# Performance work log

Hardware: AMD Instinct MI355X
Metric: run time of the kernel (lower is better)

## Reference

```python
import jax, jax.numpy as jnp
import numpy as np
from jax import lax

POINTS = 512  # number of FPS-sampled centroids
KNN = 16      # neighbors per centroid


def setup_inputs() -> dict:
    key = jax.random.key(0)
    # [B, N, 3+C]: first 3 channels are xyz coordinates, rest are features
    x = jax.random.normal(key, (8, 16384, 16), dtype=jnp.float32)
    return {"x": x}


def _furthest_point_sample(xyz, npoint):
    """Standard FPS (seeded at index 0, as in the pointnet2 CUDA op).
    xyz: [B, N, 3] -> idx: [B, npoint] int32."""
    B, N, _ = xyz.shape

    def step(carry, _):
        min_d, last = carry
        last_pt = jnp.take_along_axis(xyz, last[:, None, None], axis=1)  # [B,1,3]
        d = jnp.sum((xyz - last_pt) ** 2, axis=-1)                        # [B,N]
        min_d = jnp.minimum(min_d, d)
        nxt = jnp.argmax(min_d, axis=-1).astype(jnp.int32)
        return (min_d, nxt), nxt

    first = jnp.zeros((B,), dtype=jnp.int32)
    init = (jnp.full((B, N), 1e10, dtype=xyz.dtype), first)
    _, rest = lax.scan(step, init, None, length=npoint - 1)  # [npoint-1, B]
    return jnp.concatenate([first[:, None], rest.T], axis=1)  # [B, npoint]


def _index_points(points, idx):
    """points: [B,N,C], idx: [B,S] or [B,S,K] -> gathered [*idx.shape, C]."""
    B = points.shape[0]
    flat = idx.reshape(B, -1)                                  # [B, S*K]
    out = jnp.take_along_axis(points, flat[:, :, None], axis=1)
    return out.reshape(*idx.shape, points.shape[-1])


def reference(x):
    # FPS over coordinates only
    idx = _furthest_point_sample(x[:, :, :3], POINTS)          # [B, P]
    sampled = _index_points(x, idx)                             # [B, P, 3+C]
    s = sampled[:, :, :3]
    p = x[:, :, :3]
    # squared euclidean distance: ||s||^2 + ||p||^2 - 2 s.p  -> [B, P, N]
    dist = (jnp.sum(s * s, axis=-1)[:, :, None]
            + jnp.sum(p * p, axis=-1)[:, None, :]
            - 2.0 * jnp.einsum('bpc,bnc->bpn', s, p))
    # full argsort then slice, matching distances.argsort()[:, :, :knn]
    knn_idx = jnp.argsort(dist, axis=-1)[:, :, :KNN]            # [B, P, K]
    return _index_points(x, knn_idx)                            # [B, P, K, 3+C]
```

## Files before the change

kernel.cpp:

```cpp
#include <hip/hip_runtime.h>
#include <hip/hip_bf16.h>
#include <stdint.h>

#define B_      8
#define N_      16384
#define NPOINT  512
#define KNN_    16
#define C_      16

__device__ __forceinline__ float fmulrn(float a, float b){ return __fmul_rn(a,b); }
__device__ __forceinline__ float faddrn(float a, float b){ return __fadd_rn(a,b); }
__device__ __forceinline__ float fsubrn(float a, float b){ return __fsub_rn(a,b); }

__device__ __forceinline__ uint32_t umax_(uint32_t a, uint32_t b){ return a > b ? a : b; }

__device__ __forceinline__ uint32_t row16_max(uint32_t x){
    uint32_t t;
    t = (uint32_t)__builtin_amdgcn_update_dpp((int)x, (int)x, 0x111, 0xf, 0xf, false); x = umax_(x, t);
    t = (uint32_t)__builtin_amdgcn_update_dpp((int)x, (int)x, 0x112, 0xf, 0xf, false); x = umax_(x, t);
    t = (uint32_t)__builtin_amdgcn_update_dpp((int)x, (int)x, 0x114, 0xf, 0xf, false); x = umax_(x, t);
    t = (uint32_t)__builtin_amdgcn_update_dpp((int)x, (int)x, 0x118, 0xf, 0xf, false); x = umax_(x, t);
    return x;
}

__device__ __forceinline__ uint32_t wave_max_uniform(uint32_t x){
    x = row16_max(x);
    uint32_t a = (uint32_t)__builtin_amdgcn_readlane((int)x, 15);
    uint32_t b = (uint32_t)__builtin_amdgcn_readlane((int)x, 31);
    uint32_t c = (uint32_t)__builtin_amdgcn_readlane((int)x, 47);
    uint32_t d = (uint32_t)__builtin_amdgcn_readlane((int)x, 63);
    return umax_(umax_(a, b), umax_(c, d));
}

__device__ __forceinline__ unsigned long long quad_max_u64(unsigned long long k){
    uint32_t lo = (uint32_t)k, hi = (uint32_t)(k >> 32);
    {
        uint32_t olo = (uint32_t)__builtin_amdgcn_update_dpp((int)lo, (int)lo, 0xB1, 0xf, 0xf, false);
        uint32_t ohi = (uint32_t)__builtin_amdgcn_update_dpp((int)hi, (int)hi, 0xB1, 0xf, 0xf, false);
        bool take = (ohi > hi) || (ohi == hi && olo > lo);
        hi = take ? ohi : hi; lo = take ? olo : lo;
    }
    {
        uint32_t olo = (uint32_t)__builtin_amdgcn_update_dpp((int)lo, (int)lo, 0x4E, 0xf, 0xf, false);
        uint32_t ohi = (uint32_t)__builtin_amdgcn_update_dpp((int)hi, (int)hi, 0x4E, 0xf, 0xf, false);
        bool take = (ohi > hi) || (ohi == hi && olo > lo);
        hi = take ? ohi : hi; lo = take ? olo : lo;
    }
    return ((unsigned long long)hi << 32) | lo;
}

__global__ void prep_kernel(const float* __restrict__ x, float4* __restrict__ pts){
    int i = blockIdx.x * blockDim.x + threadIdx.x;
    if (i >= B_ * N_) return;
    const float4* x4 = (const float4*)x;
    float4 q = x4[(size_t)i * 4];
    float p2 = faddrn(faddrn(fmulrn(q.x,q.x), fmulrn(q.y,q.y)), fmulrn(q.z,q.z));
    pts[i] = make_float4(q.x, q.y, q.z, p2);
}

#define FPS_NB  4
__global__ void zero_part_kernel(unsigned long long* __restrict__ part){
    int i = blockIdx.x * blockDim.x + threadIdx.x;
    if (i < B_ * NPOINT * FPS_NB) part[i] = 0ULL;
}

#define FPS_T    1024
#define FPS_NW   (FPS_T/64)
#define SLICE    (N_ / FPS_NB)
#define SLOTS_MB (SLICE / FPS_T)

#define FOR_S4(F) F(0) F(1) F(2) F(3)

__global__ void __launch_bounds__(FPS_T)
fps_kernel_mb(const float4* __restrict__ pts, float4* __restrict__ s_out,
              unsigned long long* __restrict__ part){
    __shared__ float2   xy[SLICE];
    __shared__ uint32_t red_v[2][FPS_NW];
    __shared__ uint32_t red_i[2][FPS_NW];

    const int b    = blockIdx.x & 7;
    const int blk  = blockIdx.x >> 3;
    const int tid  = threadIdx.x;
    const int lane = tid & 63;
    const int wv   = tid >> 6;
    const int base = blk * SLICE;
    const float4* P = pts + (size_t)b * N_;
    unsigned long long* mbox = part + ((size_t)b * NPOINT) * FPS_NB;

#define DECL_S(s) float z##s, md##s;
    FOR_S4(DECL_S)
#undef DECL_S

#define INIT_S(s) { float4 q = P[base + (s) * FPS_T + tid]; \
        xy[(s) * FPS_T + tid] = make_float2(q.x, q.y); \
        z##s = q.z; md##s = 1e10f; }
    FOR_S4(INIT_S)
#undef INIT_S

    float lx, ly, lz;
    {
        float4 q0 = P[0];
        lx = q0.x; ly = q0.y; lz = q0.z;
        if (blk == 0 && tid == 0) s_out[(size_t)b * NPOINT + 0] = q0;
    }
    __syncthreads();

    for (int it = 1; it < NPOINT; ++it){
        float    bv = -1.0f;
        uint32_t bi = 0;
#define DO_S(s) { \
        float2 c = xy[(s) * FPS_T + tid]; \
        float dx = fsubrn(c.x, lx); \
        float dy = fsubrn(c.y, ly); \
        float dz = fsubrn(z##s, lz); \
        float d  = faddrn(faddrn(fmulrn(dx,dx), fmulrn(dy,dy)), fmulrn(dz,dz)); \
        md##s = fminf(md##s, d); \
        if (md##s > bv){ bv = md##s; bi = (uint32_t)(base + (s) * FPS_T + tid); } }
        FOR_S4(DO_S)
#undef DO_S

        uint32_t vb    = __float_as_uint(bv);
        uint32_t gmaxw = wave_max_uniform(vb);
        uint32_t gidxw = wave_max_uniform((vb == gmaxw) ? ~bi : 0u);
        const int par = it & 1;
        if (lane == 0){ red_v[par][wv] = gmaxw; red_i[par][wv] = gidxw; }
        __syncthreads();
        uint32_t rv = red_v[par][lane & 15];
        uint32_t ri = red_i[par][lane & 15];
        uint32_t gv = (uint32_t)__builtin_amdgcn_readlane((int)row16_max(rv), 15);
        uint32_t gn = (uint32_t)__builtin_amdgcn_readlane(
                          (int)row16_max((rv == gv) ? ri : 0u), 15);
        unsigned long long kblk = ((unsigned long long)gv << 32) | gn;

        unsigned long long* slotp = mbox + (size_t)it * FPS_NB;
        if (tid == 0)
            __hip_atomic_store(&slotp[blk], kblk, __ATOMIC_RELAXED,
                               __HIP_MEMORY_SCOPE_AGENT);
        unsigned long long v = 0;
        int guard = 0;
        for (;;){
            if (v == 0)
                v = __hip_atomic_load(&slotp[lane & 3], __ATOMIC_RELAXED,
                                      __HIP_MEMORY_SCOPE_AGENT);
            if (__all(v != 0ULL)) break;
            if (++guard > (1 << 20)) return;
        }
        unsigned long long kmax = quad_max_u64(v);
        uint32_t gi  = ~((uint32_t)kmax);
        uint32_t giu = (uint32_t)__builtin_amdgcn_readfirstlane((int)gi);
        float4 q = P[giu];
        lx = q.x; ly = q.y; lz = q.z;
        if (blk == 0 && tid == 0) s_out[(size_t)b * NPOINT + it] = q;
    }
}

#define FOR_V(F) F(0) F(1) F(2) F(3) F(4) F(5) F(6) F(7) \
                 F(8) F(9) F(10) F(11) F(12) F(13) F(14) F(15)

__global__ void __launch_bounds__(256)
__attribute__((amdgpu_waves_per_eu(4, 4)))
knn_kernel(const float* __restrict__ x,
           const float4* __restrict__ pts,
           const float4* __restrict__ s_arr,
           float* __restrict__ out){
    const int wv   = threadIdx.x >> 6;
    const int lane = threadIdx.x & 63;
    const int blk  = blockIdx.x;
    const int b    = blk >> 7;
    const int p    = ((blk & 127) << 2) | wv;

    const float4 s = s_arr[(size_t)b * NPOINT + p];
    const float sx = s.x, sy = s.y, sz = s.z, s2 = s.w;
    const float4* P = pts + (size_t)b * N_;

#define DECLV(t) unsigned long long v##t = ~0ULL;
    FOR_V(DECLV)
#undef DECLV

#define PROC(q, n) { \
        float dot = faddrn(faddrn(fmulrn(sz, (q).z), fmulrn(sy, (q).y)), fmulrn(sx, (q).x)); \
        float d = fsubrn(faddrn(s2, (q).w), fmulrn(2.0f, dot)); \
        uint32_t bits = __float_as_uint(d); \
        uint32_t key  = bits ^ (((uint32_t)((int32_t)bits >> 31)) | 0x80000000u); \
        unsigned long long c = ((unsigned long long)key << 32) | (uint32_t)(n); \
        if (c < v15){ \
            INS(0) INS(1) INS(2) INS(3) INS(4) INS(5) INS(6) INS(7) \
            INS(8) INS(9) INS(10) INS(11) INS(12) INS(13) INS(14) INS(15) \
        } }
#define INS(t) { bool lt = c < v##t; \
                 unsigned long long lo = lt ? c : v##t; \
                 unsigned long long hi = lt ? v##t : c; \
                 v##t = lo; c = hi; }

    #pragma unroll 1
    for (int j = 0; j < N_/64; j += 4){
        const int n0 = (j << 6) | lane;
        float4 q0 = P[n0];
        float4 q1 = P[n0 + 64];
        float4 q2 = P[n0 + 128];
        float4 q3 = P[n0 + 192];
        PROC(q0, n0)
        PROC(q1, n0 + 64)
        PROC(q2, n0 + 128)
        PROC(q3, n0 + 192)
    }
#undef INS
#undef PROC

    uint32_t myidx = 0;
    const int myr = lane >> 2;
    #pragma unroll 1
    for (int r = 0; r < KNN_; ++r){
        unsigned long long h = v0;
        unsigned long long g = h;
        #pragma unroll
        for (int off = 1; off < 64; off <<= 1){
            unsigned long long o = __shfl_xor(g, off, 64);
            if (o < g) g = o;
        }
        if (h == g){
            v0=v1; v1=v2; v2=v3; v3=v4; v4=v5; v5=v6; v6=v7; v7=v8;
            v8=v9; v9=v10; v10=v11; v11=v12; v12=v13; v13=v14; v14=v15;
            v15=~0ULL;
        }
        if (myr == r) myidx = (uint32_t)g;
    }

    const int c4 = lane & 3;
    const float4* X4 = (const float4*)x;
    float4 valq = X4[((size_t)b * N_ + myidx) * 4 + c4];
    float4* O4 = (float4*)out;
    O4[(((size_t)b * NPOINT + p) * KNN_ + myr) * 4 + c4] = valq;
}

extern "C" void kernel_launch(void* const* d_in, const int* in_sizes, int n_in,
                              void* d_out, int out_size, void* d_ws, size_t ws_size,
                              hipStream_t stream) {
    const float* x = (const float*)d_in[0];
    float* out = (float*)d_out;

    const size_t pts_bytes  = (size_t)B_ * N_ * sizeof(float4);
    const size_t s_bytes    = (size_t)B_ * NPOINT * sizeof(float4);
    const size_t part_bytes = (size_t)B_ * NPOINT * FPS_NB * sizeof(unsigned long long);
    if (ws_size < pts_bytes + s_bytes + part_bytes) return;
    float4* pts   = (float4*)d_ws;
    float4* s_arr = (float4*)((char*)d_ws + pts_bytes);
    unsigned long long* part =
        (unsigned long long*)((char*)d_ws + pts_bytes + s_bytes);

    prep_kernel<<<(B_*N_ + 255)/256, 256, 0, stream>>>(x, pts);
    zero_part_kernel<<<(B_*NPOINT*FPS_NB + 255)/256, 256, 0, stream>>>(part);
    fps_kernel_mb<<<B_*FPS_NB, FPS_T, 0, stream>>>(pts, s_arr, part);
    knn_kernel<<<(B_*NPOINT)/4, 256, 0, stream>>>(x, pts, s_arr, out);
}
```

Measured before the change: 1.056 ms.

## Replace FPS block barrier with per-wave global mailbox; parallelize KNN insertion

The FPS kernel no longer does an intra-block LDS reduction and __syncthreads per iteration. Each of the 64 waves per batch publishes its own argmax key to a 64-slot global mailbox, and every wave polls all 64 slots and reduces them itself. This removes the block barrier from the sequential 511-step critical path, at the cost of 16x more global atomic traffic and a wider polling set. Separately, the KNN top-16 insertion computes all comparisons up front and shifts with selects, which shortens the serial dependency chain compared with the bubble-style insert.

Measured after the change: 2.281 ms. +116.1%, slower.

```diff
diff --git a/kernel.cpp b/kernel.cpp
--- a/kernel.cpp
+++ b/kernel.cpp
@@ -32,23 +32,6 @@
     return umax_(umax_(a, b), umax_(c, d));
 }
 
-__device__ __forceinline__ unsigned long long quad_max_u64(unsigned long long k){
-    uint32_t lo = (uint32_t)k, hi = (uint32_t)(k >> 32);
-    {
-        uint32_t olo = (uint32_t)__builtin_amdgcn_update_dpp((int)lo, (int)lo, 0xB1, 0xf, 0xf, false);
-        uint32_t ohi = (uint32_t)__builtin_amdgcn_update_dpp((int)hi, (int)hi, 0xB1, 0xf, 0xf, false);
-        bool take = (ohi > hi) || (ohi == hi && olo > lo);
-        hi = take ? ohi : hi; lo = take ? olo : lo;
-    }
-    {
-        uint32_t olo = (uint32_t)__builtin_amdgcn_update_dpp((int)lo, (int)lo, 0x4E, 0xf, 0xf, false);
-        uint32_t ohi = (uint32_t)__builtin_amdgcn_update_dpp((int)hi, (int)hi, 0x4E, 0xf, 0xf, false);
-        bool take = (ohi > hi) || (ohi == hi && olo > lo);
-        hi = take ? ohi : hi; lo = take ? olo : lo;
-    }
-    return ((unsigned long long)hi << 32) | lo;
-}
-
 __global__ void prep_kernel(const float* __restrict__ x, float4* __restrict__ pts){
     int i = blockIdx.x * blockDim.x + threadIdx.x;
     if (i >= B_ * N_) return;
@@ -58,34 +41,31 @@
     pts[i] = make_float4(q.x, q.y, q.z, p2);
 }
 
-#define FPS_NB  4
+#define FPS_NB   4
+#define NWB      64
+#define MBOX_N   (B_ * NPOINT * NWB)
 __global__ void zero_part_kernel(unsigned long long* __restrict__ part){
     int i = blockIdx.x * blockDim.x + threadIdx.x;
-    if (i < B_ * NPOINT * FPS_NB) part[i] = 0ULL;
+    if (i < MBOX_N) part[i] = 0ULL;
 }
 
 #define FPS_T    1024
-#define FPS_NW   (FPS_T/64)
 #define SLICE    (N_ / FPS_NB)
-#define SLOTS_MB (SLICE / FPS_T)
-
 #define FOR_S4(F) F(0) F(1) F(2) F(3)
 
 __global__ void __launch_bounds__(FPS_T)
 fps_kernel_mb(const float4* __restrict__ pts, float4* __restrict__ s_out,
               unsigned long long* __restrict__ part){
-    __shared__ float2   xy[SLICE];
-    __shared__ uint32_t red_v[2][FPS_NW];
-    __shared__ uint32_t red_i[2][FPS_NW];
+    __shared__ float2 xy[SLICE];
 
     const int b    = blockIdx.x & 7;
     const int blk  = blockIdx.x >> 3;
     const int tid  = threadIdx.x;
     const int lane = tid & 63;
-    const int wv   = tid >> 6;
+    const int wid  = (blk << 4) | (tid >> 6);
     const int base = blk * SLICE;
     const float4* P = pts + (size_t)b * N_;
-    unsigned long long* mbox = part + ((size_t)b * NPOINT) * FPS_NB;
+    unsigned long long* mbox = part + (size_t)b * NPOINT * NWB;
 
 #define DECL_S(s) float z##s, md##s;
     FOR_S4(DECL_S)
@@ -122,40 +102,31 @@
         uint32_t vb    = __float_as_uint(bv);
         uint32_t gmaxw = wave_max_uniform(vb);
         uint32_t gidxw = wave_max_uniform((vb == gmaxw) ? ~bi : 0u);
-        const int par = it & 1;
-        if (lane == 0){ red_v[par][wv] = gmaxw; red_i[par][wv] = gidxw; }
-        __syncthreads();
-        uint32_t rv = red_v[par][lane & 15];
-        uint32_t ri = red_i[par][lane & 15];
-        uint32_t gv = (uint32_t)__builtin_amdgcn_readlane((int)row16_max(rv), 15);
-        uint32_t gn = (uint32_t)__builtin_amdgcn_readlane(
-                          (int)row16_max((rv == gv) ? ri : 0u), 15);
-        unsigned long long kblk = ((unsigned long long)gv << 32) | gn;
-
-        unsigned long long* slotp = mbox + (size_t)it * FPS_NB;
-        if (tid == 0)
-            __hip_atomic_store(&slotp[blk], kblk, __ATOMIC_RELAXED,
+        unsigned long long kw =
+            ((unsigned long long)gmaxw << 32) | gidxw;
+        unsigned long long* slot = mbox + (size_t)it * NWB;
+        if (lane == 0)
+            __hip_atomic_store(&slot[wid], kw, __ATOMIC_RELAXED,
                                __HIP_MEMORY_SCOPE_AGENT);
         unsigned long long v = 0;
         int guard = 0;
         for (;;){
             if (v == 0)
-                v = __hip_atomic_load(&slotp[lane & 3], __ATOMIC_RELAXED,
+                v = __hip_atomic_load(&slot[lane], __ATOMIC_RELAXED,
                                       __HIP_MEMORY_SCOPE_AGENT);
             if (__all(v != 0ULL)) break;
             if (++guard > (1 << 20)) return;
         }
-        unsigned long long kmax = quad_max_u64(v);
-        uint32_t gi  = ~((uint32_t)kmax);
+        uint32_t hi = (uint32_t)(v >> 32), lo = (uint32_t)v;
+        uint32_t gv = wave_max_uniform(hi);
+        uint32_t gn = wave_max_uniform((hi == gv) ? lo : 0u);
+        uint32_t gi = ~gn;
         uint32_t giu = (uint32_t)__builtin_amdgcn_readfirstlane((int)gi);
         float4 q = P[giu];
         lx = q.x; ly = q.y; lz = q.z;
         if (blk == 0 && tid == 0) s_out[(size_t)b * NPOINT + it] = q;
     }
 }
-
-#define FOR_V(F) F(0) F(1) F(2) F(3) F(4) F(5) F(6) F(7) \
-                 F(8) F(9) F(10) F(11) F(12) F(13) F(14) F(15)
 
 __global__ void __launch_bounds__(256)
 __attribute__((amdgpu_waves_per_eu(4, 4)))
@@ -173,6 +144,8 @@
     const float sx = s.x, sy = s.y, sz = s.z, s2 = s.w;
     const float4* P = pts + (size_t)b * N_;
 
+#define FOR_V(F) F(0) F(1) F(2) F(3) F(4) F(5) F(6) F(7) \
+                 F(8) F(9) F(10) F(11) F(12) F(13) F(14) F(15)
 #define DECLV(t) unsigned long long v##t = ~0ULL;
     FOR_V(DECLV)
 #undef DECLV
@@ -184,13 +157,27 @@
         uint32_t key  = bits ^ (((uint32_t)((int32_t)bits >> 31)) | 0x80000000u); \
         unsigned long long c = ((unsigned long long)key << 32) | (uint32_t)(n); \
         if (c < v15){ \
-            INS(0) INS(1) INS(2) INS(3) INS(4) INS(5) INS(6) INS(7) \
-            INS(8) INS(9) INS(10) INS(11) INS(12) INS(13) INS(14) INS(15) \
+            bool lt0=c<v0,  lt1=c<v1,  lt2=c<v2,  lt3=c<v3; \
+            bool lt4=c<v4,  lt5=c<v5,  lt6=c<v6,  lt7=c<v7; \
+            bool lt8=c<v8,  lt9=c<v9,  lt10=c<v10, lt11=c<v11; \
+            bool lt12=c<v12, lt13=c<v13, lt14=c<v14; \
+            v15 = lt14 ? v14 : c; \
+            v14 = lt14 ? (lt13 ? v13 : c) : v14; \
+            v13 = lt13 ? (lt12 ? v12 : c) : v13; \
+            v12 = lt12 ? (lt11 ? v11 : c) : v12; \
+            v11 = lt11 ? (lt10 ? v10 : c) : v11; \
+            v10 = lt10 ? (lt9  ? v9  : c) : v10; \
+            v9  = lt9  ? (lt8  ? v8  : c) : v9;  \
+            v8  = lt8  ? (lt7  ? v7  : c) : v8;  \
+            v7  = lt7  ? (lt6  ? v6  : c) : v7;  \
+            v6  = lt6  ? (lt5  ? v5  : c) : v6;  \
+            v5  = lt5  ? (lt4  ? v4  : c) : v5;  \
+            v4  = lt4  ? (lt3  ? v3  : c) : v4;  \
+            v3  = lt3  ? (lt2  ? v2  : c) : v3;  \
+            v2  = lt2  ? (lt1  ? v1  : c) : v2;  \
+            v1  = lt1  ? (lt0  ? v0  : c) : v1;  \
+            v0  = lt0  ? c : v0; \
         } }
-#define INS(t) { bool lt = c < v##t; \
-                 unsigned long long lo = lt ? c : v##t; \
-                 unsigned long long hi = lt ? v##t : c; \
-                 v##t = lo; c = hi; }
 
     #pragma unroll 1
     for (int j = 0; j < N_/64; j += 4){
@@ -204,7 +191,6 @@
         PROC(q2, n0 + 128)
         PROC(q3, n0 + 192)
     }
-#undef INS
 #undef PROC
 
     uint32_t myidx = 0;
@@ -241,7 +227,7 @@
 
     const size_t pts_bytes  = (size_t)B_ * N_ * sizeof(float4);
     const size_t s_bytes    = (size_t)B_ * NPOINT * sizeof(float4);
-    const size_t part_bytes = (size_t)B_ * NPOINT * FPS_NB * sizeof(unsigned long long);
+    const size_t part_bytes = (size_t)MBOX_N * sizeof(unsigned long long);
     if (ws_size < pts_bytes + s_bytes + part_bytes) return;
     float4* pts   = (float4*)d_ws;
     float4* s_arr = (float4*)((char*)d_ws + pts_bytes);
@@ -249,7 +235,7 @@
         (unsigned long long*)((char*)d_ws + pts_bytes + s_bytes);
 
     prep_kernel<<<(B_*N_ + 255)/256, 256, 0, stream>>>(x, pts);
-    zero_part_kernel<<<(B_*NPOINT*FPS_NB + 255)/256, 256, 0, stream>>>(part);
+    zero_part_kernel<<<(MBOX_N + 255)/256, 256, 0, stream>>>(part);
     fps_kernel_mb<<<B_*FPS_NB, FPS_T, 0, stream>>>(pts, s_arr, part);
     knn_kernel<<<(B_*NPOINT)/4, 256, 0, stream>>>(x, pts, s_arr, out);
 }
```
